# Performance work log

Hardware: AMD Instinct MI355X
Metric: run time of the kernel (lower is better)

Reference implementation:

```python
import jax, jax.numpy as jnp
import numpy as np
from jax import lax

P = 8; E = 192; D_MODEL = E + 4; D_STATE = 16; D_CONV = 4; EXPAND = 2
D_INNER = EXPAND * D_MODEL  # 392
DT_RANK = -(-D_MODEL // 16)  # 13
MAX_FREQ = 32


def silu(v):
    return v * jax.nn.sigmoid(v)


def layernorm(v, g, b, eps=1e-5):
    m = v.mean(-1, keepdims=True)
    var = v.var(-1, keepdims=True)
    return (v - m) / jnp.sqrt(var + eps) * g + b


def mamba(x, in_w, conv_w, conv_b, xp_w, dt_w, dt_b, A_log, Dp, out_w):
    # Standard mamba_ssm Mamba block. x: (B, L, d_model)
    B, L, _ = x.shape
    xz = x @ in_w.T                      # (B,L,2*d_inner)
    xi, z = jnp.split(xz, 2, axis=-1)
    # depthwise causal conv1d (torch pads d_conv-1 both sides then truncates to L)
    xc = jnp.transpose(xi, (0, 2, 1))    # (B,d_inner,L)
    xc = lax.conv_general_dilated(xc, conv_w[:, None, :], (1,), [(D_CONV - 1, 0)],
                                  dimension_numbers=('NCH', 'OIH', 'NCH'),
                                  feature_group_count=D_INNER)
    xc = silu(jnp.transpose(xc, (0, 2, 1)) + conv_b)  # (B,L,d_inner)
    x_dbl = xc @ xp_w.T                  # (B,L,dt_rank+2*d_state)
    dt = x_dbl[..., :DT_RANK]
    Bm = x_dbl[..., DT_RANK:DT_RANK + D_STATE]
    Cm = x_dbl[..., DT_RANK + D_STATE:]
    delta = jax.nn.softplus(dt @ dt_w.T + dt_b)       # (B,L,d_inner)
    A = -jnp.exp(A_log)                               # (d_inner,d_state)
    deltaA = jnp.exp(delta[..., None] * A)            # (B,L,d_inner,d_state)
    deltaBu = delta[..., None] * Bm[:, :, None, :] * xc[..., None]

    def step(h, inp):
        dA, dBu, c = inp
        h = dA * h + dBu
        return h, jnp.einsum('bdn,bn->bd', h, c)

    h0 = jnp.zeros((B, D_INNER, D_STATE), x.dtype)
    _, ys = lax.scan(step, h0, (deltaA.transpose(1, 0, 2, 3),
                                deltaBu.transpose(1, 0, 2, 3),
                                Cm.transpose(1, 0, 2)))
    y = ys.transpose(1, 0, 2) + Dp * xc
    y = y * silu(z)
    return y @ out_w.T


def _mk_mamba_params(key):
    ks = jax.random.split(key, 6)
    s = 0.05
    return dict(
        in_w=jax.random.normal(ks[0], (2 * D_INNER, D_MODEL)) * s,
        conv_w=jax.random.normal(ks[1], (D_INNER, D_CONV)) * s,
        conv_b=jnp.zeros((D_INNER,)),
        xp_w=jax.random.normal(ks[2], (DT_RANK + 2 * D_STATE, D_INNER)) * s,
        dt_w=jax.random.normal(ks[3], (D_INNER, DT_RANK)) * s,
        dt_b=jax.random.normal(ks[4], (D_INNER,)) * 0.1,
        A_log=jnp.log(jnp.broadcast_to(jnp.arange(1, D_STATE + 1, dtype=jnp.float32), (D_INNER, D_STATE)) + 0.0),
        D=jnp.ones((D_INNER,)),
        out_w=jax.random.normal(ks[5], (D_MODEL, D_INNER)) * s,
    )


def setup_inputs() -> dict:
    key = jax.random.key(0)
    k = jax.random.split(key, 8)
    inp = {
        'x': jax.random.normal(k[0], (16, 3, 256, 256), dtype=jnp.float32),
        'patch_w': jax.random.normal(k[1], (E, 3, P, P)) * 0.05,
        'patch_b': jnp.zeros((E,)),
        'pe_ln_g': jnp.ones((E,)), 'pe_ln_b': jnp.zeros((E,)),
        'blk_ln_g': jnp.ones((D_MODEL,)), 'blk_ln_b': jnp.zeros((D_MODEL,)),
        'cls_w': jax.random.normal(k[2], (1, D_MODEL)) * 0.05,
        'cls_b': jnp.zeros((1,)),
    }
    for pref, kk in (('f_', k[3]), ('b_', k[4])):
        for name, val in _mk_mamba_params(kk).items():
            inp[pref + name] = val
    return inp


def reference(x, patch_w, patch_b, pe_ln_g, pe_ln_b,
              f_in_w, f_conv_w, f_conv_b, f_xp_w, f_dt_w, f_dt_b, f_A_log, f_D, f_out_w,
              b_in_w, b_conv_w, b_conv_b, b_xp_w, b_dt_w, b_dt_b, b_A_log, b_D, b_out_w,
              blk_ln_g, blk_ln_b, cls_w, cls_b):
    B, C, H, W = x.shape
    hp, wp = H // P, W // P
    # PatchEmbed: stride==kernel conv expressed as one GEMM over patches
    xp = x.reshape(B, C, hp, P, wp, P)
    tok = jnp.einsum('bchpwq,ecpq->bhwe', xp, patch_w) + patch_b
    tok = tok.reshape(B, hp * wp, E)
    tok = silu(layernorm(tok, pe_ln_g, pe_ln_b))
    # RotaryEmbedding: concat 4 positional channels
    L = hp * wp
    scale = 2 * np.pi / MAX_FREQ
    pos = jnp.arange(L, dtype=tok.dtype)[:, None] * scale
    row = (jnp.arange(L) // MAX_FREQ).astype(tok.dtype)[:, None] * scale
    cp = jnp.concatenate([jnp.sin(pos), jnp.cos(pos), jnp.sin(row), jnp.cos(row)], axis=-1)
    h = jnp.concatenate([tok, jnp.broadcast_to(cp[None], (B, L, 4))], axis=-1)  # (B,L,196)
    # BidirectionalMambaBlock
    fo = mamba(h, f_in_w, f_conv_w, f_conv_b, f_xp_w, f_dt_w, f_dt_b, f_A_log, f_D, f_out_w)
    bo = jnp.flip(mamba(jnp.flip(h, 1), b_in_w, b_conv_w, b_conv_b, b_xp_w, b_dt_w, b_dt_b, b_A_log, b_D, b_out_w), 1)
    out = (fo + bo) * 0.5
    out = silu(layernorm(out, blk_ln_g, blk_ln_b)) + h
    # Classifier: mean pool + linear (num_classes==2 -> 1 logit)
    return out.mean(1) @ cls_w.T + cls_b
```

## Files before the change

kernel.cpp:

```cpp
#include <hip/hip_runtime.h>
#include <cstdint>
#include <cstddef>

constexpr int B_   = 16;
constexpr int L_   = 1024;
constexpr int E_   = 192;
constexpr int DM   = 196;
constexpr int DI   = 392;
constexpr int DS   = 16;
constexpr int DTR  = 13;
constexpr int NTOK = B_ * L_;
constexpr int XDW  = DTR + 2 * DS;
constexpr int CH   = B_ * DI;

constexpr int KP_XZ = 224;
constexpr int KP_OP = 416;
constexpr int KP_PW = 192;

constexpr size_t HW_SZ = (size_t)NTOK * DM;
constexpr size_t DI_SZ = (size_t)NTOK * DI;

constexpr size_t O_H     = 0;
constexpr size_t O_H16   = 3211264;
constexpr size_t O_XI_F  = 5046272;
constexpr size_t O_XI_B  = 11468800;
constexpr size_t O_Z_F   = 17891328;
constexpr size_t O_Z_B   = 24313856;
constexpr size_t O_XC_F  = 30736384;
constexpr size_t O_XC_B  = 37158912;
constexpr size_t O_DTR_F = 43581440;
constexpr size_t O_DTR_B = 43794432;
constexpr size_t O_BC_F  = 44007424;
constexpr size_t O_BC_B  = 44531712;
constexpr size_t O_YS_F  = 45056000;
constexpr size_t O_YS_B  = 48267264;
constexpr size_t O_PW16  = 51478528;
constexpr size_t O_FIN16 = 51496960;
constexpr size_t O_BIN16 = 51584768;
constexpr size_t O_FOUT16= 51672576;
constexpr size_t O_BOUT16= 51713344;

typedef _Float16 half8 __attribute__((ext_vector_type(8)));
typedef _Float16 half4v __attribute__((ext_vector_type(4)));
typedef float f32x4v __attribute__((ext_vector_type(4)));

__device__ __forceinline__ float siluf(float x) {
    return x / (1.f + __expf(-x));
}

__device__ __forceinline__ float blk_sum(float v, float* red) {
    #pragma unroll
    for (int o = 32; o > 0; o >>= 1) v += __shfl_down(v, o);
    int w = threadIdx.x >> 6;
    __syncthreads();
    if ((threadIdx.x & 63) == 0) red[w] = v;
    __syncthreads();
    return red[0] + red[1] + red[2] + red[3];
}

__global__ __launch_bounds__(256) void cvt_all(const float* __restrict__ pw,
                                               const float* __restrict__ fin,
                                               const float* __restrict__ bin,
                                               const float* __restrict__ fout,
                                               const float* __restrict__ bout,
                                               _Float16* __restrict__ dst) {
    int i = blockIdx.x * 256 + threadIdx.x;
    const float* src; int K, Kp, off;
    if (i < 36864)       { src = pw;   K = 192; Kp = 192; off = i; }
    else if (i < 212480) { src = fin;  K = 196; Kp = 224; off = i - 36864; }
    else if (i < 388096) { src = bin;  K = 196; Kp = 224; off = i - 212480; }
    else if (i < 469632) { src = fout; K = 392; Kp = 416; off = i - 388096; }
    else                 { src = bout; K = 392; Kp = 416; off = i - 469632; }
    int n = off / Kp, k = off - n * Kp;
    dst[i] = (_Float16)(k < K ? src[(size_t)n * K + k] : 0.f);
}

__global__ __launch_bounds__(256) void gather_patch(const float* __restrict__ x,
                                                    _Float16* __restrict__ Xp) {
    int i = blockIdx.x * 256 + threadIdx.x;
    int tok = i / 192, r = i - tok * 192;
    int c = r >> 6, pq = r & 63, p = pq >> 3, q = pq & 7;
    int b = tok >> 10, l = tok & 1023, hh = l >> 5, wv = l & 31;
    Xp[i] = (_Float16)x[(((size_t)(b * 3 + c) * 256 + hh * 8 + p) << 8) + wv * 8 + q];
}

template <int MODE>
__device__ __forceinline__ void mfma_core(const _Float16* __restrict__ A,
                                          const _Float16* __restrict__ W,
                                          const float* __restrict__ bias,
                                          void* __restrict__ Cv_,
                                          int N, int Kpad, int ldc,
                                          int flip, int m_blk, int n_blk) {
    const int tid = threadIdx.x;
    const int wv = tid >> 6, lane = tid & 63;
    const int col = lane & 15, quad = lane >> 4;
    const int m_base = m_blk * 128 + wv * 32;
    const int n_base = n_blk * 64;

    int r0 = m_base + col, r1 = m_base + 16 + col;
    if (flip) {
        r0 = (r0 & ~1023) + (1023 - (r0 & 1023));
        r1 = (r1 & ~1023) + (1023 - (r1 & 1023));
    }
    const _Float16* a0p = A + (size_t)r0 * Kpad + quad * 8;
    const _Float16* a1p = A + (size_t)r1 * Kpad + quad * 8;

    const _Float16* bp[4];
    bool bok[4];
    #pragma unroll
    for (int j = 0; j < 4; ++j) {
        int n = n_base + j * 16 + col;
        bok[j] = (n < N);
        bp[j] = W + (size_t)(bok[j] ? n : 0) * Kpad + quad * 8;
    }

    f32x4v acc[2][4];
    #pragma unroll
    for (int i = 0; i < 2; ++i)
        #pragma unroll
        for (int j = 0; j < 4; ++j)
            #pragma unroll
            for (int r = 0; r < 4; ++r) acc[i][j][r] = 0.f;

    half8 bzero;
    #pragma unroll
    for (int q = 0; q < 8; ++q) bzero[q] = (_Float16)0.f;

    for (int k0 = 0; k0 < Kpad; k0 += 32) {
        half8 a0 = *(const half8*)(a0p + k0);
        half8 a1 = *(const half8*)(a1p + k0);
        #pragma unroll
        for (int j = 0; j < 4; ++j) {
            half8 bv = bzero;
            if (bok[j]) bv = *(const half8*)(bp[j] + k0);
            acc[0][j] = __builtin_amdgcn_mfma_f32_16x16x32_f16(a0, bv, acc[0][j], 0, 0, 0);
            acc[1][j] = __builtin_amdgcn_mfma_f32_16x16x32_f16(a1, bv, acc[1][j], 0, 0, 0);
        }
    }

    if (MODE == 0) {
        float* C = (float*)Cv_;
        #pragma unroll
        for (int i = 0; i < 2; ++i) {
            int mrow = m_base + i * 16 + quad * 4;
            #pragma unroll
            for (int j = 0; j < 4; ++j) {
                int n = n_base + j * 16 + col;
                if (n < N) {
                    float bv = bias ? bias[n] : 0.f;
                    #pragma unroll
                    for (int r = 0; r < 4; ++r)
                        C[(size_t)(mrow + r) * ldc + n] = acc[i][j][r] + bv;
                }
            }
        }
    } else {
        const int bb = m_base >> 10;
        const int t0 = m_base & 1023;
        #pragma unroll
        for (int i = 0; i < 2; ++i) {
            int tt = t0 + i * 16 + quad * 4;
            #pragma unroll
            for (int j = 0; j < 4; ++j) {
                int n = n_base + j * 16 + col;
                if (n < N) {
                    if (MODE == 1) {
                        float4 v = {acc[i][j][0], acc[i][j][1], acc[i][j][2], acc[i][j][3]};
                        *(float4*)((float*)Cv_ + (((size_t)(bb * N + n)) << 10) + tt) = v;
                    } else {
                        half4v v;
                        #pragma unroll
                        for (int r = 0; r < 4; ++r) {
                            float xx = acc[i][j][r];
                            v[r] = (_Float16)(xx / (1.f + __expf(-xx)));
                        }
                        *(half4v*)((_Float16*)Cv_ + (((size_t)(bb * N + n)) << 10) + tt) = v;
                    }
                }
            }
        }
    }
}

__global__ __launch_bounds__(256) void mfma_patch(const _Float16* __restrict__ A,
                                                  const _Float16* __restrict__ W,
                                                  const float* __restrict__ bias,
                                                  float* __restrict__ C) {
    mfma_core<0>(A, W, bias, C, 192, KP_PW, 192, 0, blockIdx.x, blockIdx.y);
}

__global__ __launch_bounds__(256) void mfma_xz(const _Float16* __restrict__ A,
                                               const _Float16* __restrict__ Wf,
                                               const _Float16* __restrict__ Wb,
                                               float* __restrict__ C0, _Float16* __restrict__ C1,
                                               float* __restrict__ C2, _Float16* __restrict__ C3) {
    const int zi = blockIdx.z;
    const _Float16* W = (zi < 2 ? Wf : Wb) + (size_t)(zi & 1) * DI * KP_XZ;
    const int flip = zi >> 1;
    if (zi == 0)      mfma_core<1>(A, W, nullptr, C0, DI, KP_XZ, 0, flip, blockIdx.x, blockIdx.y);
    else if (zi == 1) mfma_core<3>(A, W, nullptr, C1, DI, KP_XZ, 0, flip, blockIdx.x, blockIdx.y);
    else if (zi == 2) mfma_core<1>(A, W, nullptr, C2, DI, KP_XZ, 0, flip, blockIdx.x, blockIdx.y);
    else              mfma_core<3>(A, W, nullptr, C3, DI, KP_XZ, 0, flip, blockIdx.x, blockIdx.y);
}

__global__ __launch_bounds__(256) void mfma_op(const _Float16* __restrict__ Af,
                                               const _Float16* __restrict__ Ab,
                                               const _Float16* __restrict__ Wf,
                                               const _Float16* __restrict__ Wb,
                                               float* __restrict__ Cf, float* __restrict__ Cb) {
    const int zi = blockIdx.z;
    mfma_core<0>(zi ? Ab : Af, zi ? Wb : Wf, nullptr, zi ? Cb : Cf,
                 DM, KP_OP, DM, 0, blockIdx.x, blockIdx.y);
}

__global__ __launch_bounds__(256) void ln_silu_pos(const float* __restrict__ tok,
                                                   const float* __restrict__ g,
                                                   const float* __restrict__ bb,
                                                   float* __restrict__ h,
                                                   _Float16* __restrict__ h16) {
    const int w = threadIdx.x >> 6, lane = threadIdx.x & 63;
    const int t = blockIdx.x * 4 + w;
    const float* tp = tok + (size_t)t * E_;
    float v[3];
    float s1 = 0.f, s2 = 0.f;
    #pragma unroll
    for (int i = 0; i < 3; ++i) {
        v[i] = tp[lane + i * 64];
        s1 += v[i];
        s2 = fmaf(v[i], v[i], s2);
    }
    #pragma unroll
    for (int o = 32; o > 0; o >>= 1) {
        s1 += __shfl_xor(s1, o);
        s2 += __shfl_xor(s2, o);
    }
    float mean = s1 * (1.f / E_);
    float var = s2 * (1.f / E_) - mean * mean;
    float inv = rsqrtf(var + 1e-5f);
    float* hp = h + (size_t)t * DM;
    _Float16* hq = h16 + (size_t)t * KP_XZ;
    #pragma unroll
    for (int i = 0; i < 3; ++i) {
        int e = lane + i * 64;
        float o = siluf((v[i] - mean) * inv * g[e] + bb[e]);
        hp[e] = o;
        hq[e] = (_Float16)o;
    }
    const int l = t & 1023;
    const float scale = 0.19634954084936207f;
    if (lane < 4) {
        float pv = (lane == 0) ? sinf(l * scale)
                 : (lane == 1) ? cosf(l * scale)
                 : (lane == 2) ? sinf((float)(l >> 5) * scale)
                 :               cosf((float)(l >> 5) * scale);
        hp[E_ + lane] = pv;
        hq[E_ + lane] = (_Float16)pv;
    } else if (lane < 32) {
        hq[192 + lane] = (_Float16)0.f;
    }
}

__global__ __launch_bounds__(256) void conv_silu_T(
        const float* __restrict__ xiT_f, const float* __restrict__ xiT_b,
        float* __restrict__ xcT_f, float* __restrict__ xcT_b,
        const float* __restrict__ fw, const float* __restrict__ fb,
        const float* __restrict__ bw, const float* __restrict__ bb2) {
    int i = blockIdx.x * 256 + threadIdx.x;
    int rall = i >> 8;
    int dir = rall >= CH;
    int r = rall - (dir ? CH : 0);
    int d = r % DI;
    int t0 = (i & 255) << 2;
    const float* xi = (dir ? xiT_b : xiT_f) + ((size_t)r << 10) + t0;
    float cur[4], prev[4] = {0.f, 0.f, 0.f, 0.f};
    *(float4*)cur = *(const float4*)xi;
    if (t0) *(float4*)prev = *(const float4*)(xi - 4);
    const float* w = (dir ? bw : fw) + d * 4;
    float bias = (dir ? bb2 : fb)[d];
    float xv[7] = {prev[1], prev[2], prev[3], cur[0], cur[1], cur[2], cur[3]};
    float o[4];
    #pragma unroll
    for (int tt = 0; tt < 4; ++tt) {
        float a = bias;
        #pragma unroll
        for (int k = 0; k < 4; ++k) a = fmaf(xv[tt + k], w[k], a);
        o[tt] = siluf(a);
    }
    *(float4*)((dir ? xcT_b : xcT_f) + ((size_t)r << 10) + t0) = *(float4*)o;
}

__global__ __launch_bounds__(256) void gemm_xdbl(const float* __restrict__ Af,
                                                 const float* __restrict__ Ab,
                                                 const float* __restrict__ Wf,
                                                 const float* __restrict__ Wb,
                                                 float* __restrict__ dtrf,
                                                 float* __restrict__ dtrb,
                                                 float* __restrict__ bcf,
                                                 float* __restrict__ bcb) {
    const int yi = blockIdx.y;
    const float* A = yi ? Ab : Af;
    const float* W = yi ? Wb : Wf;
    float* dtr = yi ? dtrb : dtrf;
    float* bc = yi ? bcb : bcf;
    __shared__ __align__(16) float As[16][68];
    __shared__ __align__(16) float Ws[16][68];
    const int m0 = blockIdx.x * 64;
    const int t = threadIdx.x;
    const int tx = t & 15, ty = t >> 4;
    float acc[4][4] = {};
    const int arow_l = t >> 2;
    const int kq = (t & 3) * 4;
    const int bb_ = m0 >> 10, tt0 = m0 & 1023;
    for (int kt = 0; kt < 25; ++kt) {
        const int k0 = kt << 4;
        {
            int kr = t >> 4, tc = t & 15;
            int kk = k0 + kr;
            float4 v = {0.f, 0.f, 0.f, 0.f};
            if (kk < DI)
                v = *(const float4*)(A + (((size_t)bb_ * DI + kk) << 10) + tt0 + tc * 4);
            *(float4*)&As[kr][tc * 4] = v;
        }
        {
            bool okn = arow_l < XDW;
            const float* wp = W + (size_t)arow_l * DI;
            #pragma unroll
            for (int jj = 0; jj < 4; ++jj) {
                int kk = k0 + kq + jj;
                Ws[kq + jj][arow_l] = (okn && kk < DI) ? wp[kk] : 0.f;
            }
        }
        __syncthreads();
        #pragma unroll
        for (int k = 0; k < 16; ++k) {
            float av[4], wv[4];
            *(float4*)av = *(const float4*)&As[k][ty * 4];
            *(float4*)wv = *(const float4*)&Ws[k][tx * 4];
            #pragma unroll
            for (int i = 0; i < 4; ++i)
                #pragma unroll
                for (int j = 0; j < 4; ++j)
                    acc[i][j] = fmaf(av[i], wv[j], acc[i][j]);
        }
        __syncthreads();
    }
    #pragma unroll
    for (int i = 0; i < 4; ++i) {
        int m = m0 + ty * 4 + i;
        #pragma unroll
        for (int j = 0; j < 4; ++j) {
            int n = tx * 4 + j;
            float v = acc[i][j];
            if (n < DTR) dtr[(size_t)m * DTR + n] = v;
            else if (n < XDW) bc[(size_t)m * 32 + (n - DTR)] = v;
        }
    }
}

__global__ __launch_bounds__(256) void delta_kernel(
        const float* __restrict__ dtr_f, const float* __restrict__ dtr_b,
        float* __restrict__ dlT_f, float* __restrict__ dlT_b,
        const float* __restrict__ f_dt_w, const float* __restrict__ f_dt_b,
        const float* __restrict__ b_dt_w, const float* __restrict__ b_dt_b) {
    int i = blockIdx.x * 256 + threadIdx.x;
    int dir = i >= (int)DI_SZ;
    int j = dir ? i - (int)DI_SZ : i;
    int r = j >> 10, t = j & 1023;
    int b = r / DI, d = r - (r / DI) * DI;
    size_t tok = ((size_t)b << 10) + t;
    const float* xd = (dir ? dtr_b : dtr_f) + tok * DTR;
    const float* w = (dir ? b_dt_w : f_dt_w) + d * DTR;
    float acc = (dir ? b_dt_b : f_dt_b)[d];
    #pragma unroll
    for (int q = 0; q < DTR; ++q) acc = fmaf(xd[q], w[q], acc);
    float sp = fmaxf(acc, 0.f) + log1pf(__expf(-fabsf(acc)));
    (dir ? dlT_b : dlT_f)[j] = sp;
}

__global__ __launch_bounds__(256) void scan_kernel(
        const float* __restrict__ dlT_f, const float* __restrict__ dlT_b,
        const float* __restrict__ xcT_f, const float* __restrict__ xcT_b,
        const float* __restrict__ bc_f,  const float* __restrict__ bc_b,
        const _Float16* __restrict__ zT_f, const _Float16* __restrict__ zT_b,
        _Float16* __restrict__ y16_f,    _Float16* __restrict__ y16_b,
        const float* __restrict__ fA, const float* __restrict__ bA,
        const float* __restrict__ fD, const float* __restrict__ bD) {
    __shared__ float sP[8][8][16];
    __shared__ float sH[8][8][16];
    __shared__ float sI[8][8][16];
    const int tid = threadIdx.x;
    const int ni = tid & 3;
    const int c  = (tid >> 2) & 7;
    const int ch_l = tid >> 5;
    const int chain = blockIdx.x * 8 + ch_l;
    const int dir = chain >= CH;
    const int r = chain - (dir ? CH : 0);
    const int b = r / DI, d = r - (r / DI) * DI;

    const float* dlT = (dir ? dlT_b : dlT_f) + ((size_t)r << 10);
    const float* uT  = (dir ? xcT_b : xcT_f) + ((size_t)r << 10);
    const _Float16* zT = (dir ? zT_b : zT_f) + ((size_t)r << 10);
    const float* BC  = (dir ? bc_b  : bc_f)  + (((size_t)b << 10) * 32);
    _Float16* y16    = (dir ? y16_b : y16_f) + ((size_t)r << 10);
    const float* Al  = (dir ? bA : fA) + d * DS + ni * 4;
    float Av[4];
    #pragma unroll
    for (int i = 0; i < 4; ++i) Av[i] = -__expf(Al[i]) * 1.4426950408889634f;
    const float Dd = (dir ? bD : fD)[d];
    const int t0 = c << 7;

    if (c < 7) {
        float h[4] = {0.f, 0.f, 0.f, 0.f};
        float S = 0.f;
        for (int g = 0; g < 32; ++g) {
            const int tg = t0 + g * 4;
            float4 d4 = *(const float4*)(dlT + tg);
            float4 u4 = *(const float4*)(uT + tg);
            float dv[4] = {d4.x, d4.y, d4.z, d4.w};
            float uv[4] = {u4.x, u4.y, u4.z, u4.w};
            #pragma unroll
            for (int tt = 0; tt < 4; ++tt) {
                float4 B4 = *(const float4*)(BC + (size_t)(tg + tt) * 32 + ni * 4);
                float w = dv[tt] * uv[tt];
                S += dv[tt];
                float Bv[4] = {B4.x, B4.y, B4.z, B4.w};
                #pragma unroll
                for (int i = 0; i < 4; ++i)
                    h[i] = fmaf(exp2f(dv[tt] * Av[i]), h[i], w * Bv[i]);
            }
        }
        #pragma unroll
        for (int i = 0; i < 4; ++i) {
            sP[ch_l][c][ni * 4 + i] = exp2f(S * Av[i]);
            sH[ch_l][c][ni * 4 + i] = h[i];
        }
    }
    __syncthreads();

    if (tid < 128) {
        const int ch = tid >> 4, n = tid & 15;
        float hi = 0.f;
        #pragma unroll
        for (int cc = 0; cc < 8; ++cc) {
            sI[ch][cc][n] = hi;
            if (cc < 7) hi = sH[ch][cc][n] + sP[ch][cc][n] * hi;
        }
    }
    __syncthreads();

    {
        float h[4];
        #pragma unroll
        for (int i = 0; i < 4; ++i) h[i] = sI[ch_l][c][ni * 4 + i];
        _Float16 ybuf[8] __attribute__((aligned(16)));
        half8 zb;
        for (int g = 0; g < 32; ++g) {
            if ((g & 7) == 0)
                zb = *(const half8*)(zT + t0 + ((g >> 3) << 5) + ni * 8);
            const int tg = t0 + g * 4;
            float4 d4 = *(const float4*)(dlT + tg);
            float4 u4 = *(const float4*)(uT + tg);
            float dv[4] = {d4.x, d4.y, d4.z, d4.w};
            float uv[4] = {u4.x, u4.y, u4.z, u4.w};
            float pq[4];
            #pragma unroll
            for (int tt = 0; tt < 4; ++tt) {
                float4 B4 = *(const float4*)(BC + (size_t)(tg + tt) * 32 + ni * 4);
                float4 C4 = *(const float4*)(BC + (size_t)(tg + tt) * 32 + 16 + ni * 4);
                float w = dv[tt] * uv[tt];
                float Bv[4] = {B4.x, B4.y, B4.z, B4.w};
                float Cv[4] = {C4.x, C4.y, C4.z, C4.w};
                float p = 0.f;
                #pragma unroll
                for (int i = 0; i < 4; ++i) {
                    h[i] = fmaf(exp2f(dv[tt] * Av[i]), h[i], w * Bv[i]);
                    p = fmaf(h[i], Cv[i], p);
                }
                pq[tt] = p;
            }
            #pragma unroll
            for (int tt = 0; tt < 4; ++tt) {
                pq[tt] += __shfl_xor(pq[tt], 1);
                pq[tt] += __shfl_xor(pq[tt], 2);
            }
            if (((g >> 1) & 3) == ni) {
                const int base = (g & 1) * 4;
                #pragma unroll
                for (int tt = 0; tt < 4; ++tt)
                    ybuf[base + tt] =
                        (_Float16)((pq[tt] + Dd * uv[tt]) * (float)zb[base + tt]);
            }
            if ((g & 7) == 7)
                *(half8*)(y16 + t0 + ((g >> 3) << 5) + ni * 8) = *(half8*)ybuf;
        }
    }
}

__global__ __launch_bounds__(256) void transp_y(
        const _Float16* __restrict__ yf, const _Float16* __restrict__ yb,
        _Float16* __restrict__ of, _Float16* __restrict__ ob) {
    __shared__ _Float16 tile[64][72];
    const int dblk = blockIdx.z % 7, dir = blockIdx.z / 7;
    const int b = blockIdx.y, tb = blockIdx.x;
    const _Float16* y = dir ? yb : yf;
    _Float16* o = dir ? ob : of;
    const int d0 = dblk * 64, t0 = tb * 64;
    const int dl = threadIdx.x >> 2, ts = (threadIdx.x & 3) * 16;
    const int d = d0 + dl;
    if (d < DI) {
        const _Float16* src = y + (((size_t)(b * DI + d)) << 10) + t0 + ts;
        *(half8*)&tile[dl][ts] = *(const half8*)src;
        *(half8*)&tile[dl][ts + 8] = *(const half8*)(src + 8);
    } else {
        #pragma unroll
        for (int q = 0; q < 16; ++q) tile[dl][ts + q] = (_Float16)0.f;
    }
    __syncthreads();
    const int tl = threadIdx.x >> 2, ds = (threadIdx.x & 3) * 16;
    if (d0 + ds < KP_OP) {
        _Float16 v[16] __attribute__((aligned(16)));
        #pragma unroll
        for (int q = 0; q < 16; ++q) v[q] = tile[ds + q][tl];
        _Float16* dst = o + ((size_t)((b << 10) + t0 + tl)) * KP_OP + d0 + ds;
        *(half8*)dst = *(half8*)&v[0];
        *(half8*)(dst + 8) = *(half8*)&v[8];
    }
}

__global__ __launch_bounds__(256) void final_head(
        const float* __restrict__ fo, const float* __restrict__ bo,
        const float* __restrict__ h, const float* __restrict__ g,
        const float* __restrict__ bb, const float* __restrict__ cls_w,
        float* __restrict__ partial) {
    const int w = threadIdx.x >> 6, lane = threadIdx.x & 63;
    const int t = blockIdx.x * 4 + w;
    const int b = t >> 10, l = t & 1023;
    const float* fp = fo + (size_t)t * DM;
    const float* bp = bo + ((size_t)(b << 10) + (1023 - l)) * DM;
    const float* hp = h + (size_t)t * DM;
    float v[4];
    float s1 = 0.f, s2 = 0.f;
    #pragma unroll
    for (int i = 0; i < 4; ++i) {
        int e = lane + i * 64;
        bool ok = (i < 3) || (lane < 4);
        float vv = ok ? 0.5f * (fp[e] + bp[e]) : 0.f;
        v[i] = vv;
        s1 += vv;
        s2 = fmaf(vv, vv, s2);
    }
    #pragma unroll
    for (int o = 32; o > 0; o >>= 1) {
        s1 += __shfl_xor(s1, o);
        s2 += __shfl_xor(s2, o);
    }
    float mean = s1 * (1.f / DM);
    float var = s2 * (1.f / DM) - mean * mean;
    float inv = rsqrtf(var + 1e-5f);
    float c = 0.f;
    #pragma unroll
    for (int i = 0; i < 4; ++i) {
        int e = lane + i * 64;
        bool ok = (i < 3) || (lane < 4);
        if (ok) {
            float o2 = (v[i] - mean) * inv * g[e] + bb[e];
            o2 = siluf(o2) + hp[e];
            c = fmaf(o2, cls_w[e], c);
        }
    }
    #pragma unroll
    for (int o = 32; o > 0; o >>= 1) c += __shfl_xor(c, o);
    if (lane == 0) partial[t] = c;
}

__global__ __launch_bounds__(256) void head_reduce(const float* __restrict__ partial,
                                                   const float* __restrict__ cls_b,
                                                   float* __restrict__ out) {
    __shared__ float red[4];
    const int b = blockIdx.x;
    const float* p = partial + ((size_t)b << 10);
    float s = 0.f;
    for (int i = threadIdx.x; i < 1024; i += 256) s += p[i];
    s = blk_sum(s, red);
    if (threadIdx.x == 0) out[b] = s * (1.f / 1024.f) + cls_b[0];
}

extern "C" void kernel_launch(void* const* d_in, const int* in_sizes, int n_in,
                              void* d_out, int out_size, void* d_ws, size_t ws_size,
                              hipStream_t stream) {
    const float* x        = (const float*)d_in[0];
    const float* patch_w  = (const float*)d_in[1];
    const float* patch_b  = (const float*)d_in[2];
    const float* pe_g     = (const float*)d_in[3];
    const float* pe_b     = (const float*)d_in[4];
    const float* blk_g    = (const float*)d_in[5];
    const float* blk_b    = (const float*)d_in[6];
    const float* cls_w    = (const float*)d_in[7];
    const float* cls_b    = (const float*)d_in[8];
    const float* f_in_w   = (const float*)d_in[9];
    const float* f_conv_w = (const float*)d_in[10];
    const float* f_conv_b = (const float*)d_in[11];
    const float* f_xp_w   = (const float*)d_in[12];
    const float* f_dt_w   = (const float*)d_in[13];
    const float* f_dt_b   = (const float*)d_in[14];
    const float* f_A_log  = (const float*)d_in[15];
    const float* f_D      = (const float*)d_in[16];
    const float* f_out_w  = (const float*)d_in[17];
    const float* b_in_w   = (const float*)d_in[18];
    const float* b_conv_w = (const float*)d_in[19];
    const float* b_conv_b = (const float*)d_in[20];
    const float* b_xp_w   = (const float*)d_in[21];
    const float* b_dt_w   = (const float*)d_in[22];
    const float* b_dt_b   = (const float*)d_in[23];
    const float* b_A_log  = (const float*)d_in[24];
    const float* b_D      = (const float*)d_in[25];
    const float* b_out_w  = (const float*)d_in[26];

    float* ws = (float*)d_ws;
    float* out = (float*)d_out;

    float* Hb        = ws + O_H;
    _Float16* H16    = (_Float16*)(ws + O_H16);
    float* XIf       = ws + O_XI_F;
    float* XIb       = ws + O_XI_B;
    _Float16* ZT16f  = (_Float16*)(ws + O_Z_F);
    _Float16* ZT16b  = (_Float16*)(ws + O_Z_B);
    _Float16* YsTf16 = (_Float16*)(ws + O_Z_F);
    _Float16* YsTb16 = (_Float16*)(ws + O_Z_B);
    float* XCf       = ws + O_XC_F;
    float* XCb       = ws + O_XC_B;
    float* DTRf      = ws + O_DTR_F;
    float* DTRb      = ws + O_DTR_B;
    float* BCf       = ws + O_BC_F;
    float* BCb       = ws + O_BC_B;
    _Float16* Xp16   = (_Float16*)(ws + O_YS_F);
    float* TokRaw    = ws + O_YS_B;
    _Float16* Y16f   = (_Float16*)(ws + O_YS_F);
    _Float16* Y16b   = (_Float16*)(ws + O_YS_B);
    _Float16* PW16   = (_Float16*)(ws + O_PW16);
    _Float16* FIN16  = (_Float16*)(ws + O_FIN16);
    _Float16* BIN16  = (_Float16*)(ws + O_BIN16);
    _Float16* FOUT16 = (_Float16*)(ws + O_FOUT16);
    _Float16* BOUT16 = (_Float16*)(ws + O_BOUT16);

    cvt_all<<<2153, 256, 0, stream>>>(patch_w, f_in_w, b_in_w, f_out_w, b_out_w, PW16);

    gather_patch<<<(NTOK * 192) / 256, 256, 0, stream>>>(x, Xp16);
    mfma_patch<<<dim3(NTOK / 128, 3), 256, 0, stream>>>(Xp16, PW16, patch_b, TokRaw);
    ln_silu_pos<<<NTOK / 4, 256, 0, stream>>>(TokRaw, pe_g, pe_b, Hb, H16);

    mfma_xz<<<dim3(NTOK / 128, 7, 4), 256, 0, stream>>>(H16, FIN16, BIN16,
                                                        XIf, ZT16f, XIb, ZT16b);
    conv_silu_T<<<2 * CH, 256, 0, stream>>>(XIf, XIb, XCf, XCb,
                                            f_conv_w, f_conv_b, b_conv_w, b_conv_b);
    gemm_xdbl<<<dim3(NTOK / 64, 2), 256, 0, stream>>>(XCf, XCb, f_xp_w, b_xp_w,
                                                      DTRf, DTRb, BCf, BCb);
    delta_kernel<<<(2 * (int)DI_SZ) / 256, 256, 0, stream>>>(
        DTRf, DTRb, XIf, XIb, f_dt_w, f_dt_b, b_dt_w, b_dt_b);
    scan_kernel<<<2 * CH / 8, 256, 0, stream>>>(
        XIf, XIb, XCf, XCb, BCf, BCb, ZT16f, ZT16b, Y16f, Y16b,
        f_A_log, b_A_log, f_D, b_D);
    transp_y<<<dim3(16, 16, 14), 256, 0, stream>>>(Y16f, Y16b, YsTf16, YsTb16);
    mfma_op<<<dim3(NTOK / 128, 4, 2), 256, 0, stream>>>(YsTf16, YsTb16,
                                                        FOUT16, BOUT16, XIf, XIb);
    final_head<<<NTOK / 4, 256, 0, stream>>>(XIf, XIb, Hb, blk_g, blk_b, cls_w, XCf);
    head_reduce<<<B_, 256, 0, stream>>>(XCf, cls_b, out);
}
```

Before: 522.0 us.

## Store intermediates in fp16 and fuse causal conv into x_dbl GEMM loader

The xi projection output, the out-projection outputs and the residual h are now stored in fp16 instead of fp32, and the fp32 copy of h is dropped. The separate depthwise conv+SiLU kernel is removed: the x_dbl GEMM computes the conv on the fly from fp16 xi while loading its A tile, and also writes xc out for the scan. This cuts global memory traffic and one kernel launch, at the cost of reduced precision in the intermediates and extra compute in the GEMM loader.

After: 503.0 us. 3.6% less time.

```diff
diff --git a/kernel.cpp b/kernel.cpp
--- a/kernel.cpp
+++ b/kernel.cpp
@@ -154,6 +154,21 @@
                 }
             }
         }
+    } else if (MODE == 4) {
+        _Float16* C = (_Float16*)Cv_;
+        #pragma unroll
+        for (int i = 0; i < 2; ++i) {
+            int mrow = m_base + i * 16 + quad * 4;
+            #pragma unroll
+            for (int j = 0; j < 4; ++j) {
+                int n = n_base + j * 16 + col;
+                if (n < N) {
+                    #pragma unroll
+                    for (int r = 0; r < 4; ++r)
+                        C[(size_t)(mrow + r) * ldc + n] = (_Float16)acc[i][j][r];
+                }
+            }
+        }
     } else {
         const int bb = m_base >> 10;
         const int t0 = m_base & 1023;
@@ -164,18 +179,14 @@
             for (int j = 0; j < 4; ++j) {
                 int n = n_base + j * 16 + col;
                 if (n < N) {
-                    if (MODE == 1) {
-                        float4 v = {acc[i][j][0], acc[i][j][1], acc[i][j][2], acc[i][j][3]};
-                        *(float4*)((float*)Cv_ + (((size_t)(bb * N + n)) << 10) + tt) = v;
-                    } else {
-                        half4v v;
-                        #pragma unroll
-                        for (int r = 0; r < 4; ++r) {
-                            float xx = acc[i][j][r];
-                            v[r] = (_Float16)(xx / (1.f + __expf(-xx)));
-                        }
-                        *(half4v*)((_Float16*)Cv_ + (((size_t)(bb * N + n)) << 10) + tt) = v;
+                    half4v v;
+                    #pragma unroll
+                    for (int r = 0; r < 4; ++r) {
+                        float xx = acc[i][j][r];
+                        if (MODE == 3) xx = xx / (1.f + __expf(-xx));
+                        v[r] = (_Float16)xx;
                     }
+                    *(half4v*)((_Float16*)Cv_ + (((size_t)(bb * N + n)) << 10) + tt) = v;
                 }
             }
         }
@@ -192,14 +203,14 @@
 __global__ __launch_bounds__(256) void mfma_xz(const _Float16* __restrict__ A,
                                                const _Float16* __restrict__ Wf,
                                                const _Float16* __restrict__ Wb,
-                                               float* __restrict__ C0, _Float16* __restrict__ C1,
-                                               float* __restrict__ C2, _Float16* __restrict__ C3) {
+                                               _Float16* __restrict__ C0, _Float16* __restrict__ C1,
+                                               _Float16* __restrict__ C2, _Float16* __restrict__ C3) {
     const int zi = blockIdx.z;
     const _Float16* W = (zi < 2 ? Wf : Wb) + (size_t)(zi & 1) * DI * KP_XZ;
     const int flip = zi >> 1;
-    if (zi == 0)      mfma_core<1>(A, W, nullptr, C0, DI, KP_XZ, 0, flip, blockIdx.x, blockIdx.y);
+    if (zi == 0)      mfma_core<2>(A, W, nullptr, C0, DI, KP_XZ, 0, flip, blockIdx.x, blockIdx.y);
     else if (zi == 1) mfma_core<3>(A, W, nullptr, C1, DI, KP_XZ, 0, flip, blockIdx.x, blockIdx.y);
-    else if (zi == 2) mfma_core<1>(A, W, nullptr, C2, DI, KP_XZ, 0, flip, blockIdx.x, blockIdx.y);
+    else if (zi == 2) mfma_core<2>(A, W, nullptr, C2, DI, KP_XZ, 0, flip, blockIdx.x, blockIdx.y);
     else              mfma_core<3>(A, W, nullptr, C3, DI, KP_XZ, 0, flip, blockIdx.x, blockIdx.y);
 }
 
@@ -207,16 +218,15 @@
                                                const _Float16* __restrict__ Ab,
                                                const _Float16* __restrict__ Wf,
                                                const _Float16* __restrict__ Wb,
-                                               float* __restrict__ Cf, float* __restrict__ Cb) {
+                                               _Float16* __restrict__ Cf, _Float16* __restrict__ Cb) {
     const int zi = blockIdx.z;
-    mfma_core<0>(zi ? Ab : Af, zi ? Wb : Wf, nullptr, zi ? Cb : Cf,
+    mfma_core<4>(zi ? Ab : Af, zi ? Wb : Wf, nullptr, zi ? Cb : Cf,
                  DM, KP_OP, DM, 0, blockIdx.x, blockIdx.y);
 }
 
 __global__ __launch_bounds__(256) void ln_silu_pos(const float* __restrict__ tok,
                                                    const float* __restrict__ g,
                                                    const float* __restrict__ bb,
-                                                   float* __restrict__ h,
                                                    _Float16* __restrict__ h16) {
     const int w = threadIdx.x >> 6, lane = threadIdx.x & 63;
     const int t = blockIdx.x * 4 + w;
@@ -237,13 +247,11 @@
     float mean = s1 * (1.f / E_);
     float var = s2 * (1.f / E_) - mean * mean;
     float inv = rsqrtf(var + 1e-5f);
-    float* hp = h + (size_t)t * DM;
     _Float16* hq = h16 + (size_t)t * KP_XZ;
     #pragma unroll
     for (int i = 0; i < 3; ++i) {
         int e = lane + i * 64;
         float o = siluf((v[i] - mean) * inv * g[e] + bb[e]);
-        hp[e] = o;
         hq[e] = (_Float16)o;
     }
     const int l = t & 1023;
@@ -253,55 +261,34 @@
                  : (lane == 1) ? cosf(l * scale)
                  : (lane == 2) ? sinf((float)(l >> 5) * scale)
                  :               cosf((float)(l >> 5) * scale);
-        hp[E_ + lane] = pv;
         hq[E_ + lane] = (_Float16)pv;
     } else if (lane < 32) {
         hq[192 + lane] = (_Float16)0.f;
     }
 }
 
-__global__ __launch_bounds__(256) void conv_silu_T(
-        const float* __restrict__ xiT_f, const float* __restrict__ xiT_b,
-        float* __restrict__ xcT_f, float* __restrict__ xcT_b,
-        const float* __restrict__ fw, const float* __restrict__ fb,
-        const float* __restrict__ bw, const float* __restrict__ bb2) {
-    int i = blockIdx.x * 256 + threadIdx.x;
-    int rall = i >> 8;
-    int dir = rall >= CH;
-    int r = rall - (dir ? CH : 0);
-    int d = r % DI;
-    int t0 = (i & 255) << 2;
-    const float* xi = (dir ? xiT_b : xiT_f) + ((size_t)r << 10) + t0;
-    float cur[4], prev[4] = {0.f, 0.f, 0.f, 0.f};
-    *(float4*)cur = *(const float4*)xi;
-    if (t0) *(float4*)prev = *(const float4*)(xi - 4);
-    const float* w = (dir ? bw : fw) + d * 4;
-    float bias = (dir ? bb2 : fb)[d];
-    float xv[7] = {prev[1], prev[2], prev[3], cur[0], cur[1], cur[2], cur[3]};
-    float o[4];
-    #pragma unroll
-    for (int tt = 0; tt < 4; ++tt) {
-        float a = bias;
-        #pragma unroll
-        for (int k = 0; k < 4; ++k) a = fmaf(xv[tt + k], w[k], a);
-        o[tt] = siluf(a);
-    }
-    *(float4*)((dir ? xcT_b : xcT_f) + ((size_t)r << 10) + t0) = *(float4*)o;
-}
-
-__global__ __launch_bounds__(256) void gemm_xdbl(const float* __restrict__ Af,
-                                                 const float* __restrict__ Ab,
+__global__ __launch_bounds__(256) void gemm_xdbl(const _Float16* __restrict__ xi_f,
+                                                 const _Float16* __restrict__ xi_b,
                                                  const float* __restrict__ Wf,
                                                  const float* __restrict__ Wb,
+                                                 const float* __restrict__ fcw,
+                                                 const float* __restrict__ fcb,
+                                                 const float* __restrict__ bcw,
+                                                 const float* __restrict__ bcb,
                                                  float* __restrict__ dtrf,
                                                  float* __restrict__ dtrb,
                                                  float* __restrict__ bcf,
-                                                 float* __restrict__ bcb) {
+                                                 float* __restrict__ bcb2,
+                                                 float* __restrict__ xcf,
+                                                 float* __restrict__ xcb) {
     const int yi = blockIdx.y;
-    const float* A = yi ? Ab : Af;
+    const _Float16* xi = yi ? xi_b : xi_f;
     const float* W = yi ? Wb : Wf;
+    const float* cw = yi ? bcw : fcw;
+    const float* cb = yi ? bcb : fcb;
     float* dtr = yi ? dtrb : dtrf;
-    float* bc = yi ? bcb : bcf;
+    float* bc = yi ? bcb2 : bcf;
+    float* xc = yi ? xcb : xcf;
     __shared__ __align__(16) float As[16][68];
     __shared__ __align__(16) float Ws[16][68];
     const int m0 = blockIdx.x * 64;
@@ -316,10 +303,30 @@
         {
             int kr = t >> 4, tc = t & 15;
             int kk = k0 + kr;
-            float4 v = {0.f, 0.f, 0.f, 0.f};
-            if (kk < DI)
-                v = *(const float4*)(A + (((size_t)bb_ * DI + kk) << 10) + tt0 + tc * 4);
-            *(float4*)&As[kr][tc * 4] = v;
+            float o4[4] = {0.f, 0.f, 0.f, 0.f};
+            if (kk < DI) {
+                const int tpos = tt0 + tc * 4;
+                const _Float16* xp = xi + (((size_t)(bb_ * DI + kk)) << 10) + tpos;
+                half4v cur = *(const half4v*)xp;
+                half4v prv;
+                if (tpos > 0) prv = *(const half4v*)(xp - 4);
+                else { prv[0] = prv[1] = prv[2] = prv[3] = (_Float16)0.f; }
+                float xw[7] = {(float)prv[1], (float)prv[2], (float)prv[3],
+                               (float)cur[0], (float)cur[1], (float)cur[2], (float)cur[3]};
+                float4 wv4 = *(const float4*)(cw + kk * 4);
+                float wc[4] = {wv4.x, wv4.y, wv4.z, wv4.w};
+                float bv = cb[kk];
+                #pragma unroll
+                for (int j = 0; j < 4; ++j) {
+                    float a = bv;
+                    #pragma unroll
+                    for (int q = 0; q < 4; ++q) a = fmaf(xw[j + q], wc[q], a);
+                    o4[j] = siluf(a);
+                }
+                *(float4*)(xc + (((size_t)(bb_ * DI + kk)) << 10) + tpos) =
+                    *(float4*)o4;
+            }
+            *(float4*)&As[kr][tc * 4] = *(float4*)o4;
         }
         {
             bool okn = arow_l < XDW;
@@ -528,23 +535,23 @@
 }
 
 __global__ __launch_bounds__(256) void final_head(
-        const float* __restrict__ fo, const float* __restrict__ bo,
-        const float* __restrict__ h, const float* __restrict__ g,
+        const _Float16* __restrict__ fo, const _Float16* __restrict__ bo,
+        const _Float16* __restrict__ h16, const float* __restrict__ g,
         const float* __restrict__ bb, const float* __restrict__ cls_w,
         float* __restrict__ partial) {
     const int w = threadIdx.x >> 6, lane = threadIdx.x & 63;
     const int t = blockIdx.x * 4 + w;
     const int b = t >> 10, l = t & 1023;
-    const float* fp = fo + (size_t)t * DM;
-    const float* bp = bo + ((size_t)(b << 10) + (1023 - l)) * DM;
-    const float* hp = h + (size_t)t * DM;
+    const _Float16* fp = fo + (size_t)t * DM;
+    const _Float16* bp = bo + ((size_t)(b << 10) + (1023 - l)) * DM;
+    const _Float16* hp = h16 + (size_t)t * KP_XZ;
     float v[4];
     float s1 = 0.f, s2 = 0.f;
     #pragma unroll
     for (int i = 0; i < 4; ++i) {
         int e = lane + i * 64;
         bool ok = (i < 3) || (lane < 4);
-        float vv = ok ? 0.5f * (fp[e] + bp[e]) : 0.f;
+        float vv = ok ? 0.5f * ((float)fp[e] + (float)bp[e]) : 0.f;
         v[i] = vv;
         s1 += vv;
         s2 = fmaf(vv, vv, s2);
@@ -564,7 +571,7 @@
         bool ok = (i < 3) || (lane < 4);
         if (ok) {
             float o2 = (v[i] - mean) * inv * g[e] + bb[e];
-            o2 = siluf(o2) + hp[e];
+            o2 = siluf(o2) + (float)hp[e];
             c = fmaf(o2, cls_w[e], c);
         }
     }
@@ -619,10 +626,13 @@
     float* ws = (float*)d_ws;
     float* out = (float*)d_out;
 
-    float* Hb        = ws + O_H;
     _Float16* H16    = (_Float16*)(ws + O_H16);
-    float* XIf       = ws + O_XI_F;
-    float* XIb       = ws + O_XI_B;
+    _Float16* XI16f  = (_Float16*)(ws + O_XI_F);
+    _Float16* XI16b  = (_Float16*)(ws + O_XI_B);
+    float* DLf       = ws + O_XI_F;
+    float* DLb       = ws + O_XI_B;
+    _Float16* FO16   = (_Float16*)(ws + O_XI_F);
+    _Float16* BO16   = (_Float16*)(ws + O_XI_B);
     _Float16* ZT16f  = (_Float16*)(ws + O_Z_F);
     _Float16* ZT16b  = (_Float16*)(ws + O_Z_B);
     _Float16* YsTf16 = (_Float16*)(ws + O_Z_F);
@@ -647,22 +657,21 @@
 
     gather_patch<<<(NTOK * 192) / 256, 256, 0, stream>>>(x, Xp16);
     mfma_patch<<<dim3(NTOK / 128, 3), 256, 0, stream>>>(Xp16, PW16, patch_b, TokRaw);
-    ln_silu_pos<<<NTOK / 4, 256, 0, stream>>>(TokRaw, pe_g, pe_b, Hb, H16);
+    ln_silu_pos<<<NTOK / 4, 256, 0, stream>>>(TokRaw, pe_g, pe_b, H16);
 
     mfma_xz<<<dim3(NTOK / 128, 7, 4), 256, 0, stream>>>(H16, FIN16, BIN16,
-                                                        XIf, ZT16f, XIb, ZT16b);
-    conv_silu_T<<<2 * CH, 256, 0, stream>>>(XIf, XIb, XCf, XCb,
-                                            f_conv_w, f_conv_b, b_conv_w, b_conv_b);
-    gemm_xdbl<<<dim3(NTOK / 64, 2), 256, 0, stream>>>(XCf, XCb, f_xp_w, b_xp_w,
-                                                      DTRf, DTRb, BCf, BCb);
+                                                        XI16f, ZT16f, XI16b, ZT16b);
+    gemm_xdbl<<<dim3(NTOK / 64, 2), 256, 0, stream>>>(
+        XI16f, XI16b, f_xp_w, b_xp_w, f_conv_w, f_conv_b, b_conv_w, b_conv_b,
+        DTRf, DTRb, BCf, BCb, XCf, XCb);
     delta_kernel<<<(2 * (int)DI_SZ) / 256, 256, 0, stream>>>(
-        DTRf, DTRb, XIf, XIb, f_dt_w, f_dt_b, b_dt_w, b_dt_b);
+        DTRf, DTRb, DLf, DLb, f_dt_w, f_dt_b, b_dt_w, b_dt_b);
     scan_kernel<<<2 * CH / 8, 256, 0, stream>>>(
-        XIf, XIb, XCf, XCb, BCf, BCb, ZT16f, ZT16b, Y16f, Y16b,
+        DLf, DLb, XCf, XCb, BCf, BCb, ZT16f, ZT16b, Y16f, Y16b,
         f_A_log, b_A_log, f_D, b_D);
     transp_y<<<dim3(16, 16, 14), 256, 0, stream>>>(Y16f, Y16b, YsTf16, YsTb16);
     mfma_op<<<dim3(NTOK / 128, 4, 2), 256, 0, stream>>>(YsTf16, YsTb16,
-                                                        FOUT16, BOUT16, XIf, XIb);
-    final_head<<<NTOK / 4, 256, 0, stream>>>(XIf, XIb, Hb, blk_g, blk_b, cls_w, XCf);
+                                                        FOUT16, BOUT16, FO16, BO16);
+    final_head<<<NTOK / 4, 256, 0, stream>>>(FO16, BO16, H16, blk_g, blk_b, cls_w, XCf);
     head_reduce<<<B_, 256, 0, stream>>>(XCf, cls_b, out);
 }
```
